# Kernel optimization log

Measured on AMD Instinct MI355X. Metric: run time of the kernel, lower is better.

## Reference

```python
import jax, jax.numpy as jnp
import numpy as np
import math

HEAD_DIM = 128
LAMBDA_INIT = 0.8
GN_EPS = 1e-05
NEG = -1e9


def ghostmax(scores):
    # softmax with an extra implicit zero logit (softmax-plus-one)
    m = jnp.maximum(jnp.max(scores, axis=-1, keepdims=True), 0.0)
    e = jnp.exp(scores - m)
    return e / (jnp.sum(e, axis=-1, keepdims=True) + jnp.exp(-m))


def setup_inputs() -> dict:
    key = jax.random.key(0)
    ks = jax.random.split(key, 8)
    B, H2, H, S, D = 2, 16, 8, 2048, HEAD_DIM
    return {
        "q": jax.random.normal(ks[0], (B, H2, S, D), dtype=jnp.float32),
        "k": jax.random.normal(ks[1], (B, H2, S, D), dtype=jnp.float32),
        "v": jax.random.normal(ks[2], (B, H, S, D), dtype=jnp.float32),
        "lambda_q1": 0.1 * jax.random.normal(ks[3], (D,), dtype=jnp.float32),
        "lambda_k1": 0.1 * jax.random.normal(ks[4], (D,), dtype=jnp.float32),
        "lambda_q2": 0.1 * jax.random.normal(ks[5], (D,), dtype=jnp.float32),
        "lambda_k2": 0.1 * jax.random.normal(ks[6], (D,), dtype=jnp.float32),
        "gn_weight": jnp.ones((H * D,), dtype=jnp.float32),
        "gn_bias": jnp.zeros((H * D,), dtype=jnp.float32),
    }


def reference(q, k, v, lambda_q1, lambda_k1, lambda_q2, lambda_k2, gn_weight, gn_bias):
    B, H2, S, D = q.shape
    H = H2 // 2
    scaling = 1.0 / math.sqrt(D)
    # [B, 2H, S, S] attention scores
    scores = jnp.einsum("bhsd,bhtd->bhst", q, k) * scaling
    causal_mask = jnp.triu(jnp.full((S, S), NEG, dtype=scores.dtype), k=1)
    scores = scores + causal_mask[None, None]
    w = ghostmax(scores)
    w = w.reshape(B, H, 2, S, S)
    lam = (
        jnp.exp(jnp.sum(lambda_q1 * lambda_k1))
        - jnp.exp(jnp.sum(lambda_q2 * lambda_k2))
        + LAMBDA_INIT
    )
    w = w[:, :, 0] - lam * w[:, :, 1]  # [B, H, S, S]
    out = jnp.einsum("bhst,bhtd->bhsd", w, v)  # [B, H, S, D]
    # torch .reshape(B, -1, S): raw row-major reinterpretation
    out = out.reshape(B, H * D, S)
    # GroupNorm: num_groups=H over channels H*D, normalized over (group channels, seq)
    g = out.reshape(B, H, D * S)
    mean = jnp.mean(g, axis=-1, keepdims=True)
    var = jnp.var(g, axis=-1, keepdims=True)
    g = (g - mean) * jax.lax.rsqrt(var + GN_EPS)
    out = g.reshape(B, H * D, S) * gn_weight[None, :, None] + gn_bias[None, :, None]
    return out * (1.0 - LAMBDA_INIT)
```

## Files before the change

kernel.cpp:

```cpp
#include <hip/hip_runtime.h>
#include <hip/hip_bf16.h>
#include <cstddef>
#include <cstdint>


typedef __bf16 bf16x8 __attribute__((ext_vector_type(8)));
typedef __bf16 bf16x4 __attribute__((ext_vector_type(4)));
typedef float f32x4 __attribute__((ext_vector_type(4)));

constexpr int SEQ = 2048;
constexpr int DH  = 128;
constexpr int NH  = 8;
constexpr int NH2 = 16;
constexpr float SCALE = 0.088388347648318447f;

constexpr size_t QK_ELEMS = (size_t)2 * NH2 * SEQ * DH;
constexpr size_t V_ELEMS  = (size_t)2 * NH  * SEQ * DH;
constexpr size_t OFF_KB   = 4096;
constexpr size_t OFF_VT   = OFF_KB + QK_ELEMS * 2;
constexpr size_t WS_NEED  = OFF_VT + V_ELEMS * 2;

__device__ __forceinline__ void load_lds16(const void* g, void* l) {
  __builtin_amdgcn_global_load_lds(
      (const __attribute__((address_space(1))) uint32_t*)g,
      (__attribute__((address_space(3))) uint32_t*)l, 16, 0, 0);
}

__device__ __forceinline__ bf16x8 cvt8(float4 a, float4 b) {
  bf16x8 r;
  r[0] = (__bf16)a.x; r[1] = (__bf16)a.y; r[2] = (__bf16)a.z; r[3] = (__bf16)a.w;
  r[4] = (__bf16)b.x; r[5] = (__bf16)b.y; r[6] = (__bf16)b.z; r[7] = (__bf16)b.w;
  return r;
}

__global__ __launch_bounds__(256) void prep_kernel(
    const float* __restrict__ k, const float* __restrict__ v,
    __bf16* __restrict__ Kb, __bf16* __restrict__ Vtb,
    float* __restrict__ stats)
{
  __shared__ float tile[32][33];
  const int id = blockIdx.x;
  if (id == 0 && threadIdx.x < 64) stats[threadIdx.x] = 0.f;
  if (id < 4096) {
    const size_t i = ((size_t)id * 256 + threadIdx.x) * 8;
    float4 a = *(const float4*)(k + i);
    float4 b = *(const float4*)(k + i + 4);
    *(bf16x8*)(Kb + i) = cvt8(a, b);
  } else {
    const int vid = id - 4096;
    const int tt = vid & 63, dt = (vid >> 6) & 3, bh = vid >> 8;
    const int tr = threadIdx.x >> 3, tc = (threadIdx.x & 7) * 4;
    const float* src = v + ((size_t)bh * SEQ + tt * 32) * DH + dt * 32;
    float4 f = *(const float4*)(src + (size_t)tr * DH + tc);
    tile[tr][tc + 0] = f.x; tile[tr][tc + 1] = f.y;
    tile[tr][tc + 2] = f.z; tile[tr][tc + 3] = f.w;
    __syncthreads();
    __bf16* dst = Vtb + ((size_t)bh * DH + dt * 32 + tr) * SEQ + tt * 32 + tc;
    bf16x4 o;
    o[0] = (__bf16)tile[tc + 0][tr];
    o[1] = (__bf16)tile[tc + 1][tr];
    o[2] = (__bf16)tile[tc + 2][tr];
    o[3] = (__bf16)tile[tc + 3][tr];
    *(bf16x4*)dst = o;
  }
}

__global__ __launch_bounds__(256, 2) void attn2_kernel(
    const float* __restrict__ Qf, const __bf16* __restrict__ Kb,
    const __bf16* __restrict__ Vtb,
    const float* __restrict__ lq1, const float* __restrict__ lk1,
    const float* __restrict__ lq2, const float* __restrict__ lk2,
    float* __restrict__ Obuf, float* __restrict__ stats)
{
  __shared__ __align__(16) __bf16 ldsK[2][2][32][128];
  __shared__ __align__(16) __bf16 ldsVt[2][128][32];
  __shared__ __align__(16) __bf16 ldsP[4][2][16][40];

  const int qt = (blockIdx.y < 8) ? (31 - (int)blockIdx.x) : (int)blockIdx.x;
  const int bh = blockIdx.y;
  const int b = bh >> 3, h = bh & 7;
  const int tid = threadIdx.x;
  const int w = tid >> 6, lane = tid & 63;
  const int l15 = lane & 15, quad = lane >> 4;

  float a1 = lq1[lane]*lk1[lane] + lq1[lane+64]*lk1[lane+64];
  float a2 = lq2[lane]*lk2[lane] + lq2[lane+64]*lk2[lane+64];
  #pragma unroll
  for (int off = 1; off < 64; off <<= 1) {
    a1 += __shfl_xor(a1, off);
    a2 += __shfl_xor(a2, off);
  }
  const float lam = __expf(a1) - __expf(a2) + 0.8f;

  const size_t headQK = (size_t)(b*NH2 + 2*h) * SEQ * DH;
  const float*  Qh  = Qf + headQK;
  const __bf16* Kh  = Kb + headQK;
  const __bf16* Vth = Vtb + (size_t)(b*NH + h) * DH * SEQ;

  size_t goffK[4];
  #pragma unroll
  for (int i = 0; i < 4; ++i) {
    const int R  = w*16 + i*4 + quad;
    const int sh = R >> 5, kr = R & 31;
    const int cs = lane & 15;
    goffK[i] = ((size_t)sh * SEQ + kr) * DH + ((cs ^ (kr & 15)) * 8);
  }
  size_t goffV[2];
  #pragma unroll
  for (int i = 0; i < 2; ++i) {
    const int d  = w*32 + i*16 + (lane >> 2);
    const int cs = lane & 3;
    goffV[i] = (size_t)d * SEQ + ((cs ^ (d & 3)) * 8);
  }

  __bf16* ldsKb0 = &ldsK[0][0][0][0];
  __bf16* ldsVb0 = &ldsVt[0][0][0];

  const int qb = qt * 64, nsteps = 2 * (qt + 1);

  const int qrow = qb + w*16 + l15;
  bf16x8 qf[2][4];
  #pragma unroll
  for (int sh = 0; sh < 2; ++sh) {
    const float* src = Qh + (size_t)sh*SEQ*DH + (size_t)qrow*DH + quad*8;
    #pragma unroll
    for (int kd = 0; kd < 4; ++kd) {
      float4 f0 = *(const float4*)(src + kd*32);
      float4 f1 = *(const float4*)(src + kd*32 + 4);
      f0.x *= SCALE; f0.y *= SCALE; f0.z *= SCALE; f0.w *= SCALE;
      f1.x *= SCALE; f1.y *= SCALE; f1.z *= SCALE; f1.w *= SCALE;
      qf[sh][kd] = cvt8(f0, f1);
    }
  }

  f32x4 oacc[2][8];
  float lsum[2][4];
  #pragma unroll
  for (int sh = 0; sh < 2; ++sh) {
    #pragma unroll
    for (int nt = 0; nt < 8; ++nt) oacc[sh][nt] = (f32x4){0.f,0.f,0.f,0.f};
    #pragma unroll
    for (int r = 0; r < 4; ++r) lsum[sh][r] = 0.f;
  }

  {
    const __bf16* kg = Kh;
    #pragma unroll
    for (int i = 0; i < 4; ++i)
      load_lds16(kg + goffK[i], ldsKb0 + w*2048 + i*512);
    const __bf16* vg = Vth;
    #pragma unroll
    for (int i = 0; i < 2; ++i)
      load_lds16(vg + goffV[i], ldsVb0 + w*1024 + i*512);
  }
  __syncthreads();

  for (int st = 0; st < nsteps; ++st) {
    const int cur = st & 1;
    const int kbt = st * 32;

    if (st + 1 < nsteps) {
      const int nxt = cur ^ 1;
      const __bf16* kg = Kh + (size_t)(kbt + 32) * DH;
      #pragma unroll
      for (int i = 0; i < 4; ++i)
        load_lds16(kg + goffK[i], ldsKb0 + (size_t)nxt*8192 + w*2048 + i*512);
      const __bf16* vg = Vth + (kbt + 32);
      #pragma unroll
      for (int i = 0; i < 2; ++i)
        load_lds16(vg + goffV[i], ldsVb0 + (size_t)nxt*4096 + w*1024 + i*512);
    }

    f32x4 sacc[2][2];
    #pragma unroll
    for (int sh = 0; sh < 2; ++sh)
      #pragma unroll
      for (int n = 0; n < 2; ++n)
        sacc[sh][n] = (f32x4){0.f,0.f,0.f,0.f};
    #pragma unroll
    for (int sh = 0; sh < 2; ++sh)
      #pragma unroll
      for (int n = 0; n < 2; ++n)
        #pragma unroll
        for (int kd = 0; kd < 4; ++kd) {
          bf16x8 kf = *(const bf16x8*)&ldsK[cur][sh][n*16 + l15][((kd*4 + quad) ^ l15) * 8];
          sacc[sh][n] = __builtin_amdgcn_mfma_f32_16x16x32_bf16(qf[sh][kd], kf, sacc[sh][n], 0, 0, 0);
        }

    const int qrow0 = qb + w*16 + quad*4;
    #pragma unroll
    for (int sh = 0; sh < 2; ++sh)
      #pragma unroll
      for (int r = 0; r < 4; ++r) {
        const int qr = qrow0 + r;
        const float p0 = (kbt + l15      <= qr) ? __expf(sacc[sh][0][r]) : 0.f;
        const float p1 = (kbt + l15 + 16 <= qr) ? __expf(sacc[sh][1][r]) : 0.f;
        lsum[sh][r] += p0 + p1;
        ldsP[w][sh][quad*4 + r][l15]      = (__bf16)p0;
        ldsP[w][sh][quad*4 + r][l15 + 16] = (__bf16)p1;
      }

    {
      bf16x8 pf0 = *(const bf16x8*)&ldsP[w][0][l15][quad*8];
      bf16x8 pf1 = *(const bf16x8*)&ldsP[w][1][l15][quad*8];
      #pragma unroll
      for (int nt = 0; nt < 8; ++nt) {
        bf16x8 vf = *(const bf16x8*)&ldsVt[cur][nt*16 + l15][(quad ^ (l15 & 3)) * 8];
        oacc[0][nt] = __builtin_amdgcn_mfma_f32_16x16x32_bf16(pf0, vf, oacc[0][nt], 0, 0, 0);
        oacc[1][nt] = __builtin_amdgcn_mfma_f32_16x16x32_bf16(pf1, vf, oacc[1][nt], 0, 0, 0);
      }
    }
    __syncthreads();
  }

  #pragma unroll
  for (int sh = 0; sh < 2; ++sh)
    #pragma unroll
    for (int r = 0; r < 4; ++r) {
      float vsum = lsum[sh][r];
      #pragma unroll
      for (int off = 1; off < 16; off <<= 1) vsum += __shfl_xor(vsum, off);
      lsum[sh][r] = vsum + 1.0f;
    }

  const int qrow0 = qb + w*16 + quad*4;
  float* obase = Obuf + (size_t)(b*NH + h) * SEQ * DH;
  float sum = 0.f, ss = 0.f;
  #pragma unroll
  for (int r = 0; r < 4; ++r) {
    const float i0 = 1.0f / lsum[0][r];
    const float i1 = lam / lsum[1][r];
    float* orow = obase + (size_t)(qrow0 + r) * DH + l15;
    #pragma unroll
    for (int nt = 0; nt < 8; ++nt) {
      const float val = oacc[0][nt][r] * i0 - oacc[1][nt][r] * i1;
      orow[nt*16] = val;
      sum += val;
      ss  += val * val;
    }
  }
  #pragma unroll
  for (int off = 1; off < 64; off <<= 1) {
    sum += __shfl_xor(sum, off);
    ss  += __shfl_xor(ss, off);
  }
  if (lane == 0) {
    atomicAdd(&stats[2*(b*NH + h)],     sum);
    atomicAdd(&stats[2*(b*NH + h) + 1], ss);
  }
}

__global__ __launch_bounds__(256) void attn_fb_kernel(
    const float* __restrict__ q, const float* __restrict__ k,
    const float* __restrict__ v,
    const float* __restrict__ lq1, const float* __restrict__ lk1,
    const float* __restrict__ lq2, const float* __restrict__ lk2,
    float* __restrict__ Obuf, float* __restrict__ stats)
{
  __shared__ __align__(16) __bf16 lds_k[2][32][136];
  __shared__ __align__(16) __bf16 lds_vt[128][40];
  __shared__ __align__(16) __bf16 lds_p[4][2][16][40];

  const int qt = blockIdx.x, h = blockIdx.y, b = blockIdx.z;
  const int qb = qt * 64;
  const int tid = threadIdx.x;
  const int w = tid >> 6, lane = tid & 63;
  const int l15 = lane & 15, quad = lane >> 4;

  float a1 = lq1[lane]*lk1[lane] + lq1[lane+64]*lk1[lane+64];
  float a2 = lq2[lane]*lk2[lane] + lq2[lane+64]*lk2[lane+64];
  #pragma unroll
  for (int off = 1; off < 64; off <<= 1) {
    a1 += __shfl_xor(a1, off);
    a2 += __shfl_xor(a2, off);
  }
  const float lam = __expf(a1) - __expf(a2) + 0.8f;

  const float* qh0 = q + (size_t)(b*NH2 + 2*h) * SEQ * DH;
  const float* qh1 = qh0 + (size_t)SEQ * DH;
  const float* kh0 = k + (size_t)(b*NH2 + 2*h) * SEQ * DH;
  const float* kh1 = kh0 + (size_t)SEQ * DH;
  const float* vh  = v + (size_t)(b*NH + h) * SEQ * DH;

  bf16x8 qf[2][4];
  {
    const int qrow = qb + w*16 + l15;
    #pragma unroll
    for (int sh = 0; sh < 2; ++sh) {
      const float* src = (sh ? qh1 : qh0) + (size_t)qrow * DH + quad*8;
      #pragma unroll
      for (int kd = 0; kd < 4; ++kd) {
        float4 f0 = *(const float4*)(src + kd*32);
        float4 f1 = *(const float4*)(src + kd*32 + 4);
        qf[sh][kd] = cvt8(f0, f1);
      }
    }
  }

  f32x4 oacc[2][8];
  #pragma unroll
  for (int sh = 0; sh < 2; ++sh)
    #pragma unroll
    for (int nt = 0; nt < 8; ++nt)
      oacc[sh][nt] = (f32x4){0.f,0.f,0.f,0.f};

  float mst[2][4] = {{0.f,0.f,0.f,0.f},{0.f,0.f,0.f,0.f}};
  float lst[2][4] = {{1.f,1.f,1.f,1.f},{1.f,1.f,1.f,1.f}};

  const int krow = tid >> 2, ksh = krow >> 5, kr = krow & 31;
  const int kd0 = (tid & 3) * 32;
  const float* ksrc0 = (ksh ? kh1 : kh0) + kd0;
  const int vt = tid >> 3, vd = (tid & 7) * 16;

  const int nsteps = (qb + 64) / 32;
  for (int st = 0; st < nsteps; ++st) {
    const int kbt = st * 32;
    {
      const float* sp = ksrc0 + (size_t)(kbt + kr) * DH;
      #pragma unroll
      for (int c = 0; c < 4; ++c) {
        float4 f0 = *(const float4*)(sp + c*8);
        float4 f1 = *(const float4*)(sp + c*8 + 4);
        *(bf16x8*)&lds_k[ksh][kr][kd0 + c*8] = cvt8(f0, f1);
      }
      const float* vp = vh + (size_t)(kbt + vt) * DH + vd;
      #pragma unroll
      for (int c = 0; c < 4; ++c) {
        float4 f = *(const float4*)(vp + c*4);
        lds_vt[vd + c*4 + 0][vt] = (__bf16)f.x;
        lds_vt[vd + c*4 + 1][vt] = (__bf16)f.y;
        lds_vt[vd + c*4 + 2][vt] = (__bf16)f.z;
        lds_vt[vd + c*4 + 3][vt] = (__bf16)f.w;
      }
    }
    __syncthreads();

    f32x4 sacc[2][2];
    #pragma unroll
    for (int sh = 0; sh < 2; ++sh)
      #pragma unroll
      for (int n = 0; n < 2; ++n)
        sacc[sh][n] = (f32x4){0.f,0.f,0.f,0.f};

    #pragma unroll
    for (int sh = 0; sh < 2; ++sh)
      #pragma unroll
      for (int n = 0; n < 2; ++n)
        #pragma unroll
        for (int kd = 0; kd < 4; ++kd) {
          bf16x8 bf = *(const bf16x8*)&lds_k[sh][n*16 + l15][kd*32 + quad*8];
          sacc[sh][n] = __builtin_amdgcn_mfma_f32_16x16x32_bf16(qf[sh][kd], bf, sacc[sh][n], 0, 0, 0);
        }

    const int qrow0 = qb + w*16 + quad*4;
    const int c0 = kbt + l15, c1 = c0 + 16;
    #pragma unroll
    for (int sh = 0; sh < 2; ++sh) {
      #pragma unroll
      for (int r = 0; r < 4; ++r) {
        float s0 = sacc[sh][0][r] * SCALE;
        float s1 = sacc[sh][1][r] * SCALE;
        const int qr = qrow0 + r;
        if (c0 > qr) s0 = -1e30f;
        if (c1 > qr) s1 = -1e30f;
        float mx = fmaxf(s0, s1);
        #pragma unroll
        for (int off = 1; off < 16; off <<= 1)
          mx = fmaxf(mx, __shfl_xor(mx, off));
        const float mnew = fmaxf(mst[sh][r], mx);
        const float alpha = __expf(mst[sh][r] - mnew);
        mst[sh][r] = mnew;
        const float p0 = __expf(s0 - mnew);
        const float p1 = __expf(s1 - mnew);
        float rs = p0 + p1;
        #pragma unroll
        for (int off = 1; off < 16; off <<= 1)
          rs += __shfl_xor(rs, off);
        lst[sh][r] = lst[sh][r] * alpha + rs;
        #pragma unroll
        for (int nt = 0; nt < 8; ++nt)
          oacc[sh][nt][r] *= alpha;
        lds_p[w][sh][quad*4 + r][l15]      = (__bf16)p0;
        lds_p[w][sh][quad*4 + r][l15 + 16] = (__bf16)p1;
      }
    }

    {
      bf16x8 pf0 = *(const bf16x8*)&lds_p[w][0][l15][quad*8];
      bf16x8 pf1 = *(const bf16x8*)&lds_p[w][1][l15][quad*8];
      #pragma unroll
      for (int nt = 0; nt < 8; ++nt) {
        bf16x8 vf = *(const bf16x8*)&lds_vt[nt*16 + l15][quad*8];
        oacc[0][nt] = __builtin_amdgcn_mfma_f32_16x16x32_bf16(pf0, vf, oacc[0][nt], 0, 0, 0);
        oacc[1][nt] = __builtin_amdgcn_mfma_f32_16x16x32_bf16(pf1, vf, oacc[1][nt], 0, 0, 0);
      }
    }
    __syncthreads();
  }

  const int qrow0 = qb + w*16 + quad*4;
  float* obase = Obuf + (size_t)(b*NH + h) * SEQ * DH;
  float sum = 0.f, ss = 0.f;
  #pragma unroll
  for (int r = 0; r < 4; ++r) {
    const float i0 = 1.0f / lst[0][r];
    const float i1 = lam / lst[1][r];
    float* orow = obase + (size_t)(qrow0 + r) * DH + l15;
    #pragma unroll
    for (int nt = 0; nt < 8; ++nt) {
      const float val = oacc[0][nt][r] * i0 - oacc[1][nt][r] * i1;
      orow[nt*16] = val;
      sum += val;
      ss  += val * val;
    }
  }
  #pragma unroll
  for (int off = 1; off < 64; off <<= 1) {
    sum += __shfl_xor(sum, off);
    ss  += __shfl_xor(ss, off);
  }
  if (lane == 0) {
    atomicAdd(&stats[2*(b*NH + h)],     sum);
    atomicAdd(&stats[2*(b*NH + h) + 1], ss);
  }
}

__global__ __launch_bounds__(256) void norm_kernel(
    float* __restrict__ Obuf, const float* __restrict__ stats,
    const float* __restrict__ gw, const float* __restrict__ gb)
{
  const int idx = (blockIdx.x * 256 + threadIdx.x) * 4;
  const int bh = idx >> 18;
  const int local = idx & 262143;
  const float inv = 1.0f / 262144.0f;
  const float mean = stats[2*bh] * inv;
  const float var  = stats[2*bh + 1] * inv - mean * mean;
  const float rstd = rsqrtf(var + 1e-5f);
  const int c = ((bh & 7) << 7) + (local >> 11);
  const float wq = gw[c] * rstd;
  const float bq = gb[c];
  float4 o = *(const float4*)(Obuf + idx);
  float4 r;
  r.x = ((o.x - mean) * wq + bq) * 0.2f;
  r.y = ((o.y - mean) * wq + bq) * 0.2f;
  r.z = ((o.z - mean) * wq + bq) * 0.2f;
  r.w = ((o.w - mean) * wq + bq) * 0.2f;
  *(float4*)(Obuf + idx) = r;
}

extern "C" void kernel_launch(void* const* d_in, const int* in_sizes, int n_in,
                              void* d_out, int out_size, void* d_ws, size_t ws_size,
                              hipStream_t stream) {
  const float* q   = (const float*)d_in[0];
  const float* k   = (const float*)d_in[1];
  const float* v   = (const float*)d_in[2];
  const float* lq1 = (const float*)d_in[3];
  const float* lk1 = (const float*)d_in[4];
  const float* lq2 = (const float*)d_in[5];
  const float* lk2 = (const float*)d_in[6];
  const float* gw  = (const float*)d_in[7];
  const float* gb  = (const float*)d_in[8];
  float* out = (float*)d_out;
  float* stats = (float*)d_ws;

  if (ws_size >= WS_NEED) {
    __bf16* Kb  = (__bf16*)((char*)d_ws + OFF_KB);
    __bf16* Vtb = (__bf16*)((char*)d_ws + OFF_VT);

    prep_kernel<<<8192, 256, 0, stream>>>(k, v, Kb, Vtb, stats);

    attn2_kernel<<<dim3(32, 16), 256, 0, stream>>>(q, Kb, Vtb,
        lq1, lk1, lq2, lk2, out, stats);
  } else {
    (void)hipMemsetAsync(d_ws, 0, 256, stream);
    attn_fb_kernel<<<dim3(32, NH, 2), 256, 0, stream>>>(q, k, v,
        lq1, lk1, lq2, lk2, out, stats);
  }

  const int total = 2 * NH * SEQ * DH;
  norm_kernel<<<total / 1024, 256, 0, stream>>>(out, stats, gw, gb);
}
```

Baseline: 216.5 us.

## Split KV loop across two warp groups per block with LDS reduction

Replaces the 256-thread attention kernel with a 512-thread kernel in which two 4-wave groups handle alternating 32-key tiles for the same 64-query tile, then merge their partial outputs and row sums through LDS before normalizing and writing. The grid becomes 1D and ordered longest query tiles first. This halves the serial KV loop length per block to cut the latency of the long causal tiles and improve load balance, at the cost of doubled LDS use, a final LDS merge pass, and one block per CU occupancy.

```diff
diff --git a/kernel.cpp b/kernel.cpp
--- a/kernel.cpp
+++ b/kernel.cpp
@@ -65,22 +65,25 @@
   }
 }
 
-__global__ __launch_bounds__(256, 2) void attn2_kernel(
+__global__ __launch_bounds__(512, 1) void attn3_kernel(
     const float* __restrict__ Qf, const __bf16* __restrict__ Kb,
     const __bf16* __restrict__ Vtb,
     const float* __restrict__ lq1, const float* __restrict__ lk1,
     const float* __restrict__ lq2, const float* __restrict__ lk2,
     float* __restrict__ Obuf, float* __restrict__ stats)
 {
-  __shared__ __align__(16) __bf16 ldsK[2][2][32][128];
-  __shared__ __align__(16) __bf16 ldsVt[2][128][32];
-  __shared__ __align__(16) __bf16 ldsP[4][2][16][40];
-
-  const int qt = (blockIdx.y < 8) ? (31 - (int)blockIdx.x) : (int)blockIdx.x;
-  const int bh = blockIdx.y;
+  __shared__ __align__(16) __bf16 ldsK[2][2][2][32][128];
+  __shared__ __align__(16) __bf16 ldsVt[2][2][128][32];
+  __shared__ __align__(16) __bf16 ldsP[2][4][2][16][40];
+  __shared__ float ldsL[4][2][16];
+
+  const int qt = 31 - (int)(blockIdx.x >> 4);
+  const int bh = blockIdx.x & 15;
   const int b = bh >> 3, h = bh & 7;
   const int tid = threadIdx.x;
-  const int w = tid >> 6, lane = tid & 63;
+  const int g  = tid >> 8;
+  const int t2 = tid & 255;
+  const int w = t2 >> 6, lane = tid & 63;
   const int l15 = lane & 15, quad = lane >> 4;
 
   float a1 = lq1[lane]*lk1[lane] + lq1[lane+64]*lk1[lane+64];
@@ -108,15 +111,16 @@
   size_t goffV[2];
   #pragma unroll
   for (int i = 0; i < 2; ++i) {
-    const int d  = w*32 + i*16 + (lane >> 2);
+    const int d  = w*32 + i*16 + ((t2 & 63) >> 2);
     const int cs = lane & 3;
     goffV[i] = (size_t)d * SEQ + ((cs ^ (d & 3)) * 8);
   }
 
-  __bf16* ldsKb0 = &ldsK[0][0][0][0];
-  __bf16* ldsVb0 = &ldsVt[0][0][0];
-
-  const int qb = qt * 64, nsteps = 2 * (qt + 1);
+  __bf16* ldsKg = &ldsK[g][0][0][0][0];
+  __bf16* ldsVg = &ldsVt[g][0][0][0];
+
+  const int qb = qt * 64;
+  const int nph = qt + 1;
 
   const int qrow = qb + w*16 + l15;
   bf16x8 qf[2][4];
@@ -144,31 +148,31 @@
   }
 
   {
-    const __bf16* kg = Kh;
+    const __bf16* kg = Kh + (size_t)g * 32 * DH;
     #pragma unroll
     for (int i = 0; i < 4; ++i)
-      load_lds16(kg + goffK[i], ldsKb0 + w*2048 + i*512);
-    const __bf16* vg = Vth;
+      load_lds16(kg + goffK[i], ldsKg + w*2048 + i*512);
+    const __bf16* vg = Vth + g * 32;
     #pragma unroll
     for (int i = 0; i < 2; ++i)
-      load_lds16(vg + goffV[i], ldsVb0 + w*1024 + i*512);
+      load_lds16(vg + goffV[i], ldsVg + w*1024 + i*512);
   }
   __syncthreads();
 
-  for (int st = 0; st < nsteps; ++st) {
-    const int cur = st & 1;
-    const int kbt = st * 32;
-
-    if (st + 1 < nsteps) {
+  for (int j = 0; j < nph; ++j) {
+    const int cur = j & 1;
+    const int kbt = (2*j + g) * 32;
+
+    if (j + 1 < nph) {
       const int nxt = cur ^ 1;
-      const __bf16* kg = Kh + (size_t)(kbt + 32) * DH;
+      const __bf16* kg = Kh + (size_t)(kbt + 64) * DH;
       #pragma unroll
       for (int i = 0; i < 4; ++i)
-        load_lds16(kg + goffK[i], ldsKb0 + (size_t)nxt*8192 + w*2048 + i*512);
-      const __bf16* vg = Vth + (kbt + 32);
+        load_lds16(kg + goffK[i], ldsKg + (size_t)nxt*8192 + w*2048 + i*512);
+      const __bf16* vg = Vth + (kbt + 64);
       #pragma unroll
       for (int i = 0; i < 2; ++i)
-        load_lds16(vg + goffV[i], ldsVb0 + (size_t)nxt*4096 + w*1024 + i*512);
+        load_lds16(vg + goffV[i], ldsVg + (size_t)nxt*4096 + w*1024 + i*512);
     }
 
     f32x4 sacc[2][2];
@@ -183,7 +187,7 @@
       for (int n = 0; n < 2; ++n)
         #pragma unroll
         for (int kd = 0; kd < 4; ++kd) {
-          bf16x8 kf = *(const bf16x8*)&ldsK[cur][sh][n*16 + l15][((kd*4 + quad) ^ l15) * 8];
+          bf16x8 kf = *(const bf16x8*)&ldsK[g][cur][sh][n*16 + l15][((kd*4 + quad) ^ l15) * 8];
           sacc[sh][n] = __builtin_amdgcn_mfma_f32_16x16x32_bf16(qf[sh][kd], kf, sacc[sh][n], 0, 0, 0);
         }
 
@@ -196,16 +200,16 @@
         const float p0 = (kbt + l15      <= qr) ? __expf(sacc[sh][0][r]) : 0.f;
         const float p1 = (kbt + l15 + 16 <= qr) ? __expf(sacc[sh][1][r]) : 0.f;
         lsum[sh][r] += p0 + p1;
-        ldsP[w][sh][quad*4 + r][l15]      = (__bf16)p0;
-        ldsP[w][sh][quad*4 + r][l15 + 16] = (__bf16)p1;
+        ldsP[g][w][sh][quad*4 + r][l15]      = (__bf16)p0;
+        ldsP[g][w][sh][quad*4 + r][l15 + 16] = (__bf16)p1;
       }
 
     {
-      bf16x8 pf0 = *(const bf16x8*)&ldsP[w][0][l15][quad*8];
-      bf16x8 pf1 = *(const bf16x8*)&ldsP[w][1][l15][quad*8];
+      bf16x8 pf0 = *(const bf16x8*)&ldsP[g][w][0][l15][quad*8];
+      bf16x8 pf1 = *(const bf16x8*)&ldsP[g][w][1][l15][quad*8];
       #pragma unroll
       for (int nt = 0; nt < 8; ++nt) {
-        bf16x8 vf = *(const bf16x8*)&ldsVt[cur][nt*16 + l15][(quad ^ (l15 & 3)) * 8];
+        bf16x8 vf = *(const bf16x8*)&ldsVt[g][cur][nt*16 + l15][(quad ^ (l15 & 3)) * 8];
         oacc[0][nt] = __builtin_amdgcn_mfma_f32_16x16x32_bf16(pf0, vf, oacc[0][nt], 0, 0, 0);
         oacc[1][nt] = __builtin_amdgcn_mfma_f32_16x16x32_bf16(pf1, vf, oacc[1][nt], 0, 0, 0);
       }
@@ -213,6 +217,7 @@
     __syncthreads();
   }
 
+  float lr[2][4];
   #pragma unroll
   for (int sh = 0; sh < 2; ++sh)
     #pragma unroll
@@ -220,33 +225,58 @@
       float vsum = lsum[sh][r];
       #pragma unroll
       for (int off = 1; off < 16; off <<= 1) vsum += __shfl_xor(vsum, off);
-      lsum[sh][r] = vsum + 1.0f;
-    }
-
-  const int qrow0 = qb + w*16 + quad*4;
-  float* obase = Obuf + (size_t)(b*NH + h) * SEQ * DH;
-  float sum = 0.f, ss = 0.f;
-  #pragma unroll
-  for (int r = 0; r < 4; ++r) {
-    const float i0 = 1.0f / lsum[0][r];
-    const float i1 = lam / lsum[1][r];
-    float* orow = obase + (size_t)(qrow0 + r) * DH + l15;
-    #pragma unroll
-    for (int nt = 0; nt < 8; ++nt) {
-      const float val = oacc[0][nt][r] * i0 - oacc[1][nt][r] * i1;
-      orow[nt*16] = val;
-      sum += val;
-      ss  += val * val;
-    }
-  }
-  #pragma unroll
-  for (int off = 1; off < 64; off <<= 1) {
-    sum += __shfl_xor(sum, off);
-    ss  += __shfl_xor(ss, off);
-  }
-  if (lane == 0) {
-    atomicAdd(&stats[2*(b*NH + h)],     sum);
-    atomicAdd(&stats[2*(b*NH + h) + 1], ss);
+      lr[sh][r] = vsum;
+    }
+
+  float* Oscr = (float*)&ldsK[0][0][0][0][0];
+  if (g == 1) {
+    #pragma unroll
+    for (int sh = 0; sh < 2; ++sh)
+      #pragma unroll
+      for (int nt = 0; nt < 8; ++nt)
+        #pragma unroll
+        for (int r = 0; r < 4; ++r)
+          Oscr[((w*2 + sh)*16 + quad*4 + r)*128 + nt*16 + l15] = oacc[sh][nt][r];
+    if (l15 == 0) {
+      #pragma unroll
+      for (int sh = 0; sh < 2; ++sh)
+        #pragma unroll
+        for (int r = 0; r < 4; ++r)
+          ldsL[w][sh][quad*4 + r] = lr[sh][r];
+    }
+  }
+  __syncthreads();
+
+  if (g == 0) {
+    const int qrow0 = qb + w*16 + quad*4;
+    float* obase = Obuf + (size_t)(b*NH + h) * SEQ * DH;
+    float sum = 0.f, ss = 0.f;
+    #pragma unroll
+    for (int r = 0; r < 4; ++r) {
+      const float l0 = lr[0][r] + ldsL[w][0][quad*4 + r] + 1.0f;
+      const float l1 = lr[1][r] + ldsL[w][1][quad*4 + r] + 1.0f;
+      const float i0 = 1.0f / l0;
+      const float i1 = lam / l1;
+      float* orow = obase + (size_t)(qrow0 + r) * DH + l15;
+      #pragma unroll
+      for (int nt = 0; nt < 8; ++nt) {
+        const float o0 = oacc[0][nt][r] + Oscr[((w*2 + 0)*16 + quad*4 + r)*128 + nt*16 + l15];
+        const float o1 = oacc[1][nt][r] + Oscr[((w*2 + 1)*16 + quad*4 + r)*128 + nt*16 + l15];
+        const float val = o0 * i0 - o1 * i1;
+        orow[nt*16] = val;
+        sum += val;
+        ss  += val * val;
+      }
+    }
+    #pragma unroll
+    for (int off = 1; off < 64; off <<= 1) {
+      sum += __shfl_xor(sum, off);
+      ss  += __shfl_xor(ss, off);
+    }
+    if (lane == 0) {
+      atomicAdd(&stats[2*(b*NH + h)],     sum);
+      atomicAdd(&stats[2*(b*NH + h) + 1], ss);
+    }
   }
 }
 
@@ -469,7 +499,7 @@
 
     prep_kernel<<<8192, 256, 0, stream>>>(k, v, Kb, Vtb, stats);
 
-    attn2_kernel<<<dim3(32, 16), 256, 0, stream>>>(q, Kb, Vtb,
+    attn3_kernel<<<512, 512, 0, stream>>>(q, Kb, Vtb,
         lq1, lk1, lq2, lk2, out, stats);
   } else {
     (void)hipMemsetAsync(d_ws, 0, 256, stream);
```

After: 206.8 us. 4.5% less time.
